# Kernel optimization log

Hardware: AMD Instinct MI355X
Metric: run time of the kernel (lower is better)

Reference implementation:

```python
import jax, jax.numpy as jnp
import numpy as np

C = 256          # channels
K = 7            # kernel_size
GC = 16          # group_channels
G = C // GC      # groups = 16
R = 4            # reduction_ratio
CR = C // R      # reduced channels = 64
EPS = 1e-5


def setup_inputs() -> dict:
    key = jax.random.key(0)
    ks = jax.random.split(key, 8)
    B, H, W = 8, 56, 56
    x = jax.random.normal(ks[0], (B, C, H, W), dtype=jnp.float32)
    # conv1: 1x1, C -> C//R
    W1 = jax.random.normal(ks[1], (CR, C), dtype=jnp.float32) * (1.0 / np.sqrt(C))
    b1 = jax.random.normal(ks[2], (CR,), dtype=jnp.float32) * 0.01
    # batchnorm (eval-mode) params
    gamma = jnp.ones((CR,), dtype=jnp.float32)
    beta = jnp.zeros((CR,), dtype=jnp.float32)
    mean = jax.random.normal(ks[3], (CR,), dtype=jnp.float32) * 0.1
    var = jax.random.uniform(ks[4], (CR,), dtype=jnp.float32, minval=0.5, maxval=1.5)
    # conv2: 1x1, C//R -> K*K*G
    W2 = jax.random.normal(ks[5], (K * K * G, CR), dtype=jnp.float32) * (1.0 / np.sqrt(CR))
    b2 = jax.random.normal(ks[6], (K * K * G,), dtype=jnp.float32) * 0.01
    return {"x": x, "W1": W1, "b1": b1, "gamma": gamma, "beta": beta,
            "mean": mean, "var": var, "W2": W2, "b2": b2}


def reference(x, W1, b1, gamma, beta, mean, var, W2, b2):
    B, _, H, Wd = x.shape
    pad = (K - 1) // 2
    # --- weight generation branch: conv1 -> BN(eval) -> ReLU -> conv2 ---
    y = jnp.einsum('bchw,oc->bohw', x, W1) + b1[None, :, None, None]
    y = (y - mean[None, :, None, None]) * (gamma[None, :, None, None]
        * jax.lax.rsqrt(var + EPS)[None, :, None, None]) + beta[None, :, None, None]
    y = jax.nn.relu(y)
    wgt = jnp.einsum('bchw,oc->bohw', y, W2) + b2[None, :, None, None]  # (B, G*K*K, H, W)
    wgt = wgt.reshape(B, G, K * K, H, Wd)
    # --- unfold: gather KxK neighborhoods (stride=1, same padding) ---
    xp = jnp.pad(x, ((0, 0), (0, 0), (pad, pad), (pad, pad)))
    # (B, C, K*K, H, W); kernel positions ordered row-major like nn.Unfold
    patches = jnp.stack([xp[:, :, i:i + H, j:j + Wd]
                         for i in range(K) for j in range(K)], axis=2)
    patches = patches.reshape(B, G, GC, K * K, H, Wd)
    # --- per-pixel weighted sum over kernel window ---
    out = jnp.einsum('bgckhw,bgkhw->bgchw', patches, wgt)
    return out.reshape(B, C, H, Wd)
```

## Files before the change

### kernel.cpp

```cpp
#include <hip/hip_runtime.h>
#include <hip/hip_bf16.h>

#define CCH   256
#define NG    16
#define GCN   16
#define CRD   64
#define HH    56
#define WWD   56
#define HWP   3136
#define BB    8
#define NPIX  25088
#define K2    49
#define O2N   784
#define EPSV  1e-5f

#define XROWS 62
#define XRW   64
#define CHSTR 3968

#define WLS   228

typedef unsigned short ushort_t;
typedef __attribute__((ext_vector_type(8))) short bf16x8;
typedef __attribute__((ext_vector_type(4))) float f32x4;

#define XP_OFF   0
#define XP2_SZ   8126464
#define XT_OFF   8126464
#define YT_OFF   11337728
#define W1B_OFF  12140544
#define W2B_OFF  12148736
#define B2P_OFF  12174336
#define BNS_OFF  12175136
#define BNT_OFF  12175200

__device__ __forceinline__ ushort_t f2bf(float f) {
    unsigned u = __builtin_bit_cast(unsigned, f);
    return (ushort_t)((u + 0x7FFFu + ((u >> 16) & 1u)) >> 16);
}

__global__ __launch_bounds__(256) void prep_kernel(const float* __restrict__ W1,
                                                   const float* __restrict__ b1,
                                                   const float* __restrict__ gamma,
                                                   const float* __restrict__ beta,
                                                   const float* __restrict__ mean,
                                                   const float* __restrict__ var,
                                                   const float* __restrict__ W2,
                                                   const float* __restrict__ b2,
                                                   float* __restrict__ ws) {
    int gid = blockIdx.x * 256 + threadIdx.x;
    int stride = gridDim.x * 256;
    uint4 z = {0u, 0u, 0u, 0u};
    uint4* xpv = (uint4*)(ws + XP_OFF);
    for (int e = gid; e < XP2_SZ / 4; e += stride) xpv[e] = z;

    ushort_t* w1b = (ushort_t*)(ws + W1B_OFF);
    if (gid < CRD * CCH) w1b[gid] = f2bf(W1[gid]);
    ushort_t* w2b = (ushort_t*)(ws + W2B_OFF);
    if (gid < 800 * CRD) w2b[gid] = (gid < O2N * CRD) ? f2bf(W2[gid]) : (ushort_t)0;
    if (gid < 800) ws[B2P_OFF + gid] = (gid < O2N) ? b2[gid] : 0.f;
    if (gid < CRD) {
        float s = gamma[gid] * rsqrtf(var[gid] + EPSV);
        ws[BNS_OFF + gid] = s;
        ws[BNT_OFF + gid] = (b1[gid] - mean[gid]) * s + beta[gid];
    }
}

__global__ __launch_bounds__(256) void pack_x(const float* __restrict__ x,
                                              float* __restrict__ ws) {
    __shared__ ushort_t st[64 * 270];
    int tid = threadIdx.x;
    int b = blockIdx.y, hw0 = blockIdx.x * 64;
    int lane = tid & 63, c4 = tid >> 6;
    int hw = hw0 + lane;
    int h = hw / WWD, w = hw - h * WWD;
    const float* xb = x + (b * CCH) * HWP + hw;
    float* xpd = ws + XP_OFF + (size_t)(b * CCH) * CHSTR + (h + 3) * XRW + (w + 3);
#pragma unroll 8
    for (int i = 0; i < 64; ++i) {
        int c = i * 4 + c4;
        float v = xb[c * HWP];
        st[lane * 270 + c] = f2bf(v);
        xpd[c * CHSTR] = v;
    }
    __syncthreads();
    const unsigned* stu = (const unsigned*)st;
    unsigned* xtu = (unsigned*)(ws + XT_OFF);
    int rowg = b * HWP + hw0;
#pragma unroll
    for (int k = 0; k < 32; ++k) {
        int idx = k * 256 + tid;
        int row = idx >> 7, c2 = idx & 127;
        xtu[(rowg + row) * 128 + c2] = stu[row * 135 + c2];
    }
}

__global__ __launch_bounds__(256) void conv1_mfma(float* __restrict__ ws) {
    const ushort_t* xt  = (const ushort_t*)(ws + XT_OFF);
    const ushort_t* w1b = (const ushort_t*)(ws + W1B_OFF);
    const float* bns = ws + BNS_OFF;
    const float* bnt = ws + BNT_OFF;
    ushort_t* yt = (ushort_t*)(ws + YT_OFF);

    int tid = threadIdx.x, lane = tid & 63, wv = tid >> 6;
    int lr = lane & 15, lg = lane >> 4;
    int ot = blockIdx.x;
    int pixbase = blockIdx.y * 128 + wv * 32;

    const bf16x8* ap = (const bf16x8*)(w1b + (ot * 16 + lr) * CCH + lg * 8);
    bf16x8 a[8];
#pragma unroll
    for (int ks = 0; ks < 8; ++ks) a[ks] = ap[ks * 4];

    f32x4 acc[2] = {{0.f,0.f,0.f,0.f}, {0.f,0.f,0.f,0.f}};
#pragma unroll
    for (int f = 0; f < 2; ++f) {
        const bf16x8* bp = (const bf16x8*)(xt + (pixbase + f * 16 + lr) * CCH + lg * 8);
#pragma unroll
        for (int ks = 0; ks < 8; ++ks)
            acc[f] = __builtin_amdgcn_mfma_f32_16x16x32_bf16(a[ks], bp[ks * 4], acc[f], 0, 0, 0);
    }

    int o0 = ot * 16 + lg * 4;
    float4 s4 = *(const float4*)(bns + o0);
    float4 t4 = *(const float4*)(bnt + o0);
#pragma unroll
    for (int f = 0; f < 2; ++f) {
        int pix = pixbase + f * 16 + lr;
        union { ushort_t u[4]; uint2 v; } pk;
        pk.u[0] = f2bf(fmaxf(acc[f][0] * s4.x + t4.x, 0.f));
        pk.u[1] = f2bf(fmaxf(acc[f][1] * s4.y + t4.y, 0.f));
        pk.u[2] = f2bf(fmaxf(acc[f][2] * s4.z + t4.z, 0.f));
        pk.u[3] = f2bf(fmaxf(acc[f][3] * s4.w + t4.w, 0.f));
        *(uint2*)(yt + pix * CRD + o0) = pk.v;
    }
}

__global__ __launch_bounds__(256, 3) void invol_fused(const float* __restrict__ ws,
                                                      float* __restrict__ out) {
    __shared__ uint4 lds4[2794];
    unsigned char* ldsb = (unsigned char*)lds4;

    int h0t = blockIdx.x;
    int g   = blockIdx.y;
    int b   = blockIdx.z;
    int tid = threadIdx.x, lane = tid & 63, wv = tid >> 6;
    int lr = lane & 15, lg = lane >> 4;
    int pix0 = b * HWP + h0t * 224;

    const uint4* ysrc = (const uint4*)((const ushort_t*)(ws + YT_OFF) + (size_t)pix0 * CRD);
    for (int i = tid; i < 1792; i += 256) {
        int row = i >> 3;
        unsigned off = (unsigned)(i * 16) ^ (unsigned)((row & 7) << 4);
        *(uint4*)(ldsb + off) = ysrc[i];
    }
    __syncthreads();

    const ushort_t* w2b = (const ushort_t*)(ws + W2B_OFF);
    const bf16x8* ar = (const bf16x8*)(w2b + (g * K2 + wv * 16 + lr) * CRD);
    bf16x8 a0 = ar[lg], a1 = ar[4 + lg];

    f32x4 acc[14];
#pragma unroll
    for (int pt = 0; pt < 14; ++pt) acc[pt] = (f32x4){0.f, 0.f, 0.f, 0.f};
#pragma unroll
    for (int pt = 0; pt < 14; ++pt) {
        int row = pt * 16 + lr;
        unsigned sw = (unsigned)((row & 7) << 4);
        uint4 b0 = *(const uint4*)(ldsb + ((unsigned)(row * 128 + lg * 16) ^ sw));
        uint4 b1 = *(const uint4*)(ldsb + ((unsigned)(row * 128 + 64 + lg * 16) ^ sw));
        acc[pt] = __builtin_amdgcn_mfma_f32_16x16x32_bf16(a0, __builtin_bit_cast(bf16x8, b0), acc[pt], 0, 0, 0);
        acc[pt] = __builtin_amdgcn_mfma_f32_16x16x32_bf16(a1, __builtin_bit_cast(bf16x8, b1), acc[pt], 0, 0, 0);
    }
    __syncthreads();

    float* wlf = (float*)ldsb;
    const float* b2p = ws + B2P_OFF;
    float b2v[4];
#pragma unroll
    for (int j = 0; j < 4; ++j)
        b2v[j] = b2p[g * K2 + wv * 16 + lg * 4 + j];
#pragma unroll
    for (int pt = 0; pt < 14; ++pt) {
        int pix = pt * 16 + lr;
        int r = pix / WWD;
        int w = pix - r * WWD;
#pragma unroll
        for (int j = 0; j < 4; ++j) {
            int k = wv * 16 + lg * 4 + j;
            if (k < K2)
                wlf[k * WLS + r * WWD + w] = acc[pt][j] + b2v[j];
        }
    }
    __syncthreads();

    int c4 = lane >> 4, wb = lane & 15;
    if (wb < 14) {
        int ch = g * GCN + wv * 4 + c4;
        const float* xrb = ws + XP_OFF + (size_t)(b * CCH + ch) * CHSTR
                         + (h0t * 4) * XRW + wb * 4;
        const float* wbp = wlf + wb * 4;

        f32x4 acc2[4] = {{0.f,0.f,0.f,0.f},{0.f,0.f,0.f,0.f},
                         {0.f,0.f,0.f,0.f},{0.f,0.f,0.f,0.f}};

#define XVe(e) ((e) < 4 ? xu[(e) & 3] : ((e) < 8 ? xm[(e) & 3] : xq[(e) & 3]))
#pragma unroll
        for (int xr = 0; xr < 10; ++xr) {
            f32x4 xu, xm, xq;
            __builtin_memcpy(&xu, xrb + xr * XRW, 16);
            __builtin_memcpy(&xm, xrb + xr * XRW + 4, 16);
            __builtin_memcpy(&xq, xrb + xr * XRW + 8, 16);
#pragma unroll
            for (int ki = 0; ki < 7; ++ki) {
                int r = xr - ki;
                if (r >= 0 && r < 4) {
#pragma unroll
                    for (int dj = 0; dj < 7; ++dj) {
                        int k = ki * 7 + dj;
                        f32x4 wr = *(const f32x4*)(wbp + k * WLS + r * WWD);
#pragma unroll
                        for (int t = 0; t < 4; ++t)
                            acc2[r][t] = fmaf(XVe(t + dj), wr[t], acc2[r][t]);
                    }
                }
            }
        }
#undef XVe

        float* ob = out + (size_t)(b * CCH + ch) * HWP + (h0t * 4) * WWD + wb * 4;
#pragma unroll
        for (int r = 0; r < 4; ++r) {
            float4 v = {acc2[r][0], acc2[r][1], acc2[r][2], acc2[r][3]};
            *(float4*)(ob + r * WWD) = v;
        }
    }
}

extern "C" void kernel_launch(void* const* d_in, const int* in_sizes, int n_in,
                              void* d_out, int out_size, void* d_ws, size_t ws_size,
                              hipStream_t stream) {
    const float* x     = (const float*)d_in[0];
    const float* W1    = (const float*)d_in[1];
    const float* b1    = (const float*)d_in[2];
    const float* gamma = (const float*)d_in[3];
    const float* beta  = (const float*)d_in[4];
    const float* mean  = (const float*)d_in[5];
    const float* var   = (const float*)d_in[6];
    const float* W2    = (const float*)d_in[7];
    const float* b2    = (const float*)d_in[8];

    float* ws  = (float*)d_ws;
    float* out = (float*)d_out;

    prep_kernel<<<2048, 256, 0, stream>>>(W1, b1, gamma, beta, mean, var, W2, b2, ws);
    pack_x<<<dim3(HWP / 64, BB), 256, 0, stream>>>(x, ws);
    conv1_mfma<<<dim3(4, NPIX / 128), 256, 0, stream>>>(ws);
    invol_fused<<<dim3(14, NG, BB), 256, 0, stream>>>(ws, out);
}
```

Baseline: 74.93 us.

## Zero only padding borders, read y directly, store bf16 involution weights, reorder grid

The prep kernel now zeroes only the halo rows and columns of the padded x buffer instead of the whole buffer. The involution kernel drops the LDS staging of reduced features and feeds the MFMA straight from global memory. The generated per-pixel weights are stored in LDS as bf16 in a layout that packs each 4x4 pixel tile contiguously, which cuts LDS footprint and read traffic. The x rows are loaded progressively into a register window, and the grid order is swapped so groups vary fastest. Storing weights in bf16 adds rounding error, and the larger register window may raise register pressure.

```diff
diff --git a/kernel.cpp b/kernel.cpp
--- a/kernel.cpp
+++ b/kernel.cpp
@@ -17,8 +17,6 @@
 #define XROWS 62
 #define XRW   64
 #define CHSTR 3968
-
-#define WLS   228
 
 typedef unsigned short ushort_t;
 typedef __attribute__((ext_vector_type(8))) short bf16x8;
@@ -52,7 +50,22 @@
     int stride = gridDim.x * 256;
     uint4 z = {0u, 0u, 0u, 0u};
     uint4* xpv = (uint4*)(ws + XP_OFF);
-    for (int e = gid; e < XP2_SZ / 4; e += stride) xpv[e] = z;
+    for (int e = gid; e < 2048 * 192; e += stride) {
+        int plane = e / 192, s = e - plane * 192;
+        int row, c4i;
+        if (s < 24) {
+            int rr = s >> 2;
+            row = rr < 3 ? rr : rr + 56;
+            c4i = s & 3;
+        } else {
+            int s2 = s - 24;
+            int rw = s2 / 3;
+            int m  = s2 - rw * 3;
+            row = 3 + rw;
+            c4i = (m == 0) ? 0 : 13 + m;
+        }
+        xpv[plane * 992 + row * 16 + c4i] = z;
+    }
 
     ushort_t* w1b = (ushort_t*)(ws + W1B_OFF);
     if (gid < CRD * CCH) w1b[gid] = f2bf(W1[gid]);
@@ -138,24 +151,16 @@
 
 __global__ __launch_bounds__(256, 3) void invol_fused(const float* __restrict__ ws,
                                                       float* __restrict__ out) {
-    __shared__ uint4 lds4[2794];
-    unsigned char* ldsb = (unsigned char*)lds4;
-
-    int h0t = blockIdx.x;
-    int g   = blockIdx.y;
+    __shared__ __align__(16) ushort_t wl16[K2 * 384];
+
+    int g   = blockIdx.x;
+    int h0t = blockIdx.y;
     int b   = blockIdx.z;
     int tid = threadIdx.x, lane = tid & 63, wv = tid >> 6;
     int lr = lane & 15, lg = lane >> 4;
     int pix0 = b * HWP + h0t * 224;
 
-    const uint4* ysrc = (const uint4*)((const ushort_t*)(ws + YT_OFF) + (size_t)pix0 * CRD);
-    for (int i = tid; i < 1792; i += 256) {
-        int row = i >> 3;
-        unsigned off = (unsigned)(i * 16) ^ (unsigned)((row & 7) << 4);
-        *(uint4*)(ldsb + off) = ysrc[i];
-    }
-    __syncthreads();
-
+    const ushort_t* yt  = (const ushort_t*)(ws + YT_OFF);
     const ushort_t* w2b = (const ushort_t*)(ws + W2B_OFF);
     const bf16x8* ar = (const bf16x8*)(w2b + (g * K2 + wv * 16 + lr) * CRD);
     bf16x8 a0 = ar[lg], a1 = ar[4 + lg];
@@ -165,16 +170,11 @@
     for (int pt = 0; pt < 14; ++pt) acc[pt] = (f32x4){0.f, 0.f, 0.f, 0.f};
 #pragma unroll
     for (int pt = 0; pt < 14; ++pt) {
-        int row = pt * 16 + lr;
-        unsigned sw = (unsigned)((row & 7) << 4);
-        uint4 b0 = *(const uint4*)(ldsb + ((unsigned)(row * 128 + lg * 16) ^ sw));
-        uint4 b1 = *(const uint4*)(ldsb + ((unsigned)(row * 128 + 64 + lg * 16) ^ sw));
-        acc[pt] = __builtin_amdgcn_mfma_f32_16x16x32_bf16(a0, __builtin_bit_cast(bf16x8, b0), acc[pt], 0, 0, 0);
-        acc[pt] = __builtin_amdgcn_mfma_f32_16x16x32_bf16(a1, __builtin_bit_cast(bf16x8, b1), acc[pt], 0, 0, 0);
-    }
-    __syncthreads();
-
-    float* wlf = (float*)ldsb;
+        const bf16x8* bp = (const bf16x8*)(yt + (size_t)(pix0 + pt * 16 + lr) * CRD + lg * 8);
+        acc[pt] = __builtin_amdgcn_mfma_f32_16x16x32_bf16(a0, bp[0], acc[pt], 0, 0, 0);
+        acc[pt] = __builtin_amdgcn_mfma_f32_16x16x32_bf16(a1, bp[4], acc[pt], 0, 0, 0);
+    }
+
     const float* b2p = ws + B2P_OFF;
     float b2v[4];
 #pragma unroll
@@ -185,11 +185,12 @@
         int pix = pt * 16 + lr;
         int r = pix / WWD;
         int w = pix - r * WWD;
+        int wb = w >> 2, t = w & 3;
 #pragma unroll
         for (int j = 0; j < 4; ++j) {
             int k = wv * 16 + lg * 4 + j;
             if (k < K2)
-                wlf[k * WLS + r * WWD + w] = acc[pt][j] + b2v[j];
+                wl16[k * 384 + wb * 24 + r * 4 + t] = f2bf(acc[pt][j] + b2v[j]);
         }
     }
     __syncthreads();
@@ -199,34 +200,51 @@
         int ch = g * GCN + wv * 4 + c4;
         const float* xrb = ws + XP_OFF + (size_t)(b * CCH + ch) * CHSTR
                          + (h0t * 4) * XRW + wb * 4;
-        const float* wbp = wlf + wb * 4;
+        const char* wkb = (const char*)wl16 + wb * 48;
 
         f32x4 acc2[4] = {{0.f,0.f,0.f,0.f},{0.f,0.f,0.f,0.f},
                          {0.f,0.f,0.f,0.f},{0.f,0.f,0.f,0.f}};
-
-#define XVe(e) ((e) < 4 ? xu[(e) & 3] : ((e) < 8 ? xm[(e) & 3] : xq[(e) & 3]))
-#pragma unroll
-        for (int xr = 0; xr < 10; ++xr) {
-            f32x4 xu, xm, xq;
-            __builtin_memcpy(&xu, xrb + xr * XRW, 16);
-            __builtin_memcpy(&xm, xrb + xr * XRW + 4, 16);
-            __builtin_memcpy(&xq, xrb + xr * XRW + 8, 16);
-#pragma unroll
-            for (int ki = 0; ki < 7; ++ki) {
-                int r = xr - ki;
-                if (r >= 0 && r < 4) {
-#pragma unroll
-                    for (int dj = 0; dj < 7; ++dj) {
-                        int k = ki * 7 + dj;
-                        f32x4 wr = *(const f32x4*)(wbp + k * WLS + r * WWD);
-#pragma unroll
-                        for (int t = 0; t < 4; ++t)
-                            acc2[r][t] = fmaf(XVe(t + dj), wr[t], acc2[r][t]);
-                    }
-                }
+        f32x4 xw[10][3];
+#pragma unroll
+        for (int n = 0; n < 4; ++n) {
+            __builtin_memcpy(&xw[n][0], xrb + n * XRW, 16);
+            __builtin_memcpy(&xw[n][1], xrb + n * XRW + 4, 16);
+            __builtin_memcpy(&xw[n][2], xrb + n * XRW + 8, 16);
+        }
+
+#define CV0(u) __builtin_bit_cast(float, (unsigned)((u) << 16))
+#define CV1(u) __builtin_bit_cast(float, (unsigned)((u) & 0xffff0000u))
+#define XV(row, e) ((e) < 4 ? xw[row][0][(e)] : ((e) < 8 ? xw[row][1][(e)-4] : xw[row][2][(e)-8]))
+#define FMAR(r, ua, ub)                                                   \
+    acc2[r][0] = fmaf(XV((r) + ki, dj + 0), CV0(ua), acc2[r][0]);          \
+    acc2[r][1] = fmaf(XV((r) + ki, dj + 1), CV1(ua), acc2[r][1]);          \
+    acc2[r][2] = fmaf(XV((r) + ki, dj + 2), CV0(ub), acc2[r][2]);          \
+    acc2[r][3] = fmaf(XV((r) + ki, dj + 3), CV1(ub), acc2[r][3]);
+
+#pragma unroll
+        for (int ki = 0; ki < 7; ++ki) {
+            if (ki < 6) {
+                int n = ki + 4;
+                __builtin_memcpy(&xw[n][0], xrb + n * XRW, 16);
+                __builtin_memcpy(&xw[n][1], xrb + n * XRW + 4, 16);
+                __builtin_memcpy(&xw[n][2], xrb + n * XRW + 8, 16);
             }
-        }
-#undef XVe
+#pragma unroll
+            for (int dj = 0; dj < 7; ++dj) {
+                int k = ki * 7 + dj;
+                const uint4* wp = (const uint4*)(wkb + k * 768);
+                uint4 lo = wp[0];
+                uint4 hi = wp[1];
+                FMAR(0, lo.x, lo.y)
+                FMAR(1, lo.z, lo.w)
+                FMAR(2, hi.x, hi.y)
+                FMAR(3, hi.z, hi.w)
+            }
+        }
+#undef FMAR
+#undef XV
+#undef CV0
+#undef CV1
 
         float* ob = out + (size_t)(b * CCH + ch) * HWP + (h0t * 4) * WWD + wb * 4;
 #pragma unroll
@@ -253,8 +271,8 @@
     float* ws  = (float*)d_ws;
     float* out = (float*)d_out;
 
-    prep_kernel<<<2048, 256, 0, stream>>>(W1, b1, gamma, beta, mean, var, W2, b2, ws);
+    prep_kernel<<<1536, 256, 0, stream>>>(W1, b1, gamma, beta, mean, var, W2, b2, ws);
     pack_x<<<dim3(HWP / 64, BB), 256, 0, stream>>>(x, ws);
     conv1_mfma<<<dim3(4, NPIX / 128), 256, 0, stream>>>(ws);
-    invol_fused<<<dim3(14, NG, BB), 256, 0, stream>>>(ws, out);
-}
+    invol_fused<<<dim3(NG, 14, BB), 256, 0, stream>>>(ws, out);
+}
```

New measurement: 99.73 us. +33.1%, slower.
